# Kernel optimization log

Hardware: AMD Instinct MI355X
Metric: run time of the kernel (lower is better)

Reference implementation:

```python
import jax, jax.numpy as jnp
import numpy as np

B, Hm, Wm, Dm = 1, 32, 32, 32
N = Hm * Wm * Dm
C = 128
HEADS, DH = 8, 16
G = 32
L = 2
OUT = 1


def _ln(x, g, b):
    mu = jnp.mean(x, -1, keepdims=True)
    var = jnp.mean((x - mu) ** 2, -1, keepdims=True)
    return (x - mu) * jax.lax.rsqrt(var + 1e-5) * g + b


def setup_inputs() -> dict:
    key = jax.random.key(0)
    ks = iter(jax.random.split(key, 64))
    def nrm(shape, s=0.02):
        return jax.random.normal(next(ks), shape, jnp.float32) * s
    return {
        "x": jax.random.normal(next(ks), (B, N, 3), jnp.float32),
        "fx": jax.random.normal(next(ks), (B, N, 1), jnp.float32),
        "pre_w1": nrm((4, 2 * C)), "pre_b1": jnp.zeros((2 * C,), jnp.float32),
        "pre_w2": nrm((2 * C, C)), "pre_b2": jnp.zeros((C,), jnp.float32),
        "placeholder": jax.random.uniform(next(ks), (C,), jnp.float32) / C,
        "ln1_g": jnp.ones((L, C), jnp.float32), "ln1_b": jnp.zeros((L, C), jnp.float32),
        "convx_w": nrm((L, C, C, 3, 3, 3)), "convx_b": jnp.zeros((L, C), jnp.float32),
        "convfx_w": nrm((L, C, C, 3, 3, 3)), "convfx_b": jnp.zeros((L, C), jnp.float32),
        "slice_w": nrm((L, DH, G), 0.1), "slice_b": jnp.zeros((L, G), jnp.float32),
        "temperature": jnp.full((L, 1, HEADS, 1, 1), 0.5, jnp.float32),
        "wq": nrm((L, DH, DH), 0.1), "wk": nrm((L, DH, DH), 0.1), "wv": nrm((L, DH, DH), 0.1),
        "wo": nrm((L, HEADS * DH, C)), "bo": jnp.zeros((L, C), jnp.float32),
        "ln2_g": jnp.ones((L, C), jnp.float32), "ln2_b": jnp.zeros((L, C), jnp.float32),
        "mlp_w1": nrm((L, C, C)), "mlp_b1": jnp.zeros((L, C), jnp.float32),
        "mlp_w2": nrm((L, C, C)), "mlp_b2": jnp.zeros((L, C), jnp.float32),
        "ln3_g": jnp.ones((C,), jnp.float32), "ln3_b": jnp.zeros((C,), jnp.float32),
        "out_w": nrm((C, OUT)), "out_b": jnp.zeros((OUT,), jnp.float32),
    }


def _conv3d(x, w, b):
    # x: [B,C,H,W,D], w: [O,I,3,3,3], SAME padding (kernel//2) as torch Conv3d
    y = jax.lax.conv_general_dilated(x, w, (1, 1, 1), "SAME",
                                     dimension_numbers=("NCDHW", "OIDHW", "NCDHW"))
    return y + b[None, :, None, None, None]


def _physics_attn(z, cw_x, cb_x, cw_fx, cb_fx, sw, sb, temp, wq, wk, wv, wo, bo):
    # z: [B, N, C] -> structured mesh conv projections -> slice attention
    xg = z.reshape(B, Hm, Wm, Dm, C).transpose(0, 4, 1, 2, 3)  # [B,C,H,W,D]

    def split_heads(t):  # [B,I,H,W,D] -> [B,heads,N,dh]
        return t.transpose(0, 2, 3, 4, 1).reshape(B, N, HEADS, DH).transpose(0, 2, 1, 3)

    x_mid = split_heads(_conv3d(xg, cw_x, cb_x))
    fx_mid = split_heads(_conv3d(xg, cw_fx, cb_fx))
    # slice assignment weights: [B,heads,N,G], temperature-scaled softmax
    slice_logits = (x_mid @ sw + sb) / temp
    swt = jax.nn.softmax(slice_logits, axis=-1)
    norm = jnp.sum(swt, axis=2)  # [B,heads,G]
    tok = jnp.einsum("bhnc,bhng->bhgc", fx_mid, swt) / (norm + 1e-5)[..., None]
    q, k, v = tok @ wq, tok @ wk, tok @ wv  # [B,heads,G,dh]
    attn = jax.nn.softmax((q @ k.transpose(0, 1, 3, 2)) * (DH ** -0.5), axis=-1)
    ot = attn @ v  # [B,heads,G,dh]
    out = jnp.einsum("bhgc,bhng->bhnc", ot, swt)  # de-slice back to tokens
    out = out.transpose(0, 2, 1, 3).reshape(B, N, HEADS * DH)
    return out @ wo + bo


def reference(x, fx, pre_w1, pre_b1, pre_w2, pre_b2, placeholder,
              ln1_g, ln1_b, convx_w, convx_b, convfx_w, convfx_b,
              slice_w, slice_b, temperature, wq, wk, wv, wo, bo,
              ln2_g, ln2_b, mlp_w1, mlp_b1, mlp_w2, mlp_b2,
              ln3_g, ln3_b, out_w, out_b):
    h = jnp.concatenate([x, fx], axis=-1)  # [B,N,space+fun]
    z = jax.nn.gelu(h @ pre_w1 + pre_b1, approximate=False) @ pre_w2 + pre_b2 + placeholder
    for l in range(L):
        zn = _ln(z, ln1_g[l], ln1_b[l])
        z = _physics_attn(zn, convx_w[l], convx_b[l], convfx_w[l], convfx_b[l],
                          slice_w[l], slice_b[l], temperature[l],
                          wq[l], wk[l], wv[l], wo[l], bo[l]) + z
        zn = _ln(z, ln2_g[l], ln2_b[l])
        z = jax.nn.gelu(zn @ mlp_w1[l] + mlp_b1[l], approximate=False) @ mlp_w2[l] + mlp_b2[l] + z
    return _ln(z, ln3_g, ln3_b) @ out_w + out_b
```

## Files before the change

### kernel.cpp

```cpp
#include <hip/hip_runtime.h>
#include <hip/hip_bf16.h>

#define DEV __device__ __forceinline__

constexpr int N   = 32768;
constexpr int TOTAL_IN = 2038481;

constexpr int OFF_X        = 0;
constexpr int OFF_FX       = 98304;
constexpr int OFF_PRE_W1   = 131072;
constexpr int OFF_PRE_B1   = 132096;
constexpr int OFF_PRE_W2   = 132352;
constexpr int OFF_PRE_B2   = 165120;
constexpr int OFF_PLACE    = 165248;
constexpr int OFF_LN1_G    = 165376;
constexpr int OFF_LN1_B    = 165632;
constexpr int OFF_CONVX_W  = 165888;
constexpr int OFF_CONVX_B  = 1050624;
constexpr int OFF_CONVFX_W = 1050880;
constexpr int OFF_CONVFX_B = 1935616;
constexpr int OFF_SLICE_W  = 1935872;
constexpr int OFF_SLICE_B  = 1936896;
constexpr int OFF_TEMP     = 1936960;
constexpr int OFF_WQ       = 1936976;
constexpr int OFF_WK       = 1937488;
constexpr int OFF_WV       = 1938000;
constexpr int OFF_WO       = 1938512;
constexpr int OFF_BO       = 1971280;
constexpr int OFF_LN2_G    = 1971536;
constexpr int OFF_LN2_B    = 1971792;
constexpr int OFF_MLP_W1   = 1972048;
constexpr int OFF_MLP_B1   = 2004816;
constexpr int OFF_MLP_W2   = 2005072;
constexpr int OFF_MLP_B2   = 2037840;
constexpr int OFF_LN3_G    = 2038096;
constexpr int OFF_LN3_B    = 2038224;
constexpr int OFF_OUT_W    = 2038352;
constexpr int OFF_OUT_B    = 2038480;

__device__ __constant__ int d_PRE[32] = {
  0, 98304, 131072, 132096, 132352, 165120, 165248, 165376, 165632,
  165888, 1050624, 1050880, 1935616, 1935872, 1936896, 1936960, 1936976,
  1937488, 1938000, 1938512, 1971280, 1971536, 1971792, 1972048, 2004816,
  2005072, 2037840, 2038096, 2038224, 2038352, 2038480, 2038481
};

constexpr size_t F_IN   = 16;
constexpr size_t F_WT   = 2038512;
constexpr size_t F_Z    = F_WT   + 1769472;
constexpr size_t F_ZN   = F_Z    + 4194304;
constexpr size_t F_CONV = F_ZN   + 4194304;
constexpr size_t F_SWT  = F_CONV + 8388608;
constexpr size_t F_TOKP = F_SWT  + 8388608;
constexpr size_t F_TOK2 = F_TOKP + 1114112;
constexpr size_t F_OT   = F_TOK2 + 34816;
constexpr size_t F_WP   = F_OT   + 4096;
constexpr size_t F_END  = F_WP   + 65536;

struct InPtrs { const void* p[31]; };

typedef short short8v  __attribute__((ext_vector_type(8)));
typedef float float4v  __attribute__((ext_vector_type(4)));
#define MFMA16(A,B,C) __builtin_amdgcn_mfma_f32_16x16x32_bf16(A,B,C,0,0,0)

DEV float geluf(float x) { return 0.5f * x * (1.0f + erff(x * 0.70710678118654752f)); }
DEV short f2bs(float x) { union { __hip_bfloat16 h; short s; } c; c.h = __float2bfloat16(x); return c.s; }

__global__ void k_convert(InPtrs ptrs, float* __restrict__ ws) {
  const unsigned tw = *(const unsigned*)ptrs.p[15];
  const bool isbf = (tw == 0x3F003F00u);
  int stride = gridDim.x * blockDim.x;
  for (int e = blockIdx.x * blockDim.x + threadIdx.x; e < TOTAL_IN; e += stride) {
    if ((e >= OFF_CONVX_W && e < OFF_CONVX_B) || (e >= OFF_CONVFX_W && e < OFF_CONVFX_B)) continue;
    int lo = 0, hi = 30;
#pragma unroll
    for (int it = 0; it < 5; ++it) {
      int mid = (lo + hi + 1) >> 1;
      if (e >= d_PRE[mid]) lo = mid; else hi = mid - 1;
    }
    int loc = e - d_PRE[lo];
    float v;
    if (isbf) {
      unsigned short u = ((const unsigned short*)ptrs.p[lo])[loc];
      unsigned uu = ((unsigned)u) << 16;
      v = __uint_as_float(uu);
    } else {
      v = ((const float*)ptrs.p[lo])[loc];
    }
    ws[F_IN + e] = v;
  }
}

__global__ void k_wtrans(const void* __restrict__ cwxr, const void* __restrict__ cwfr,
                         const void* __restrict__ tempraw, short* __restrict__ wtf) {
  const bool isbf = (*(const unsigned*)tempraw == 0x3F003F00u);
  int f = blockIdx.x * 256 + threadIdx.x;
  if (f >= 221184) return;
  int lane = f & 63;
  int rest = f >> 6;
  int ntile = rest & 15;
  int r2 = rest >> 4;
  int layer = r2 / 108;
  int kt = r2 - layer * 108;
  int icb = kt / 27, tap = kt - icb * 27;
  int oc = ntile * 16 + (lane & 15);
  int ic0 = icb * 32 + (lane >> 4) * 8;
  const void* cw = (oc < 128) ? cwxr : cwfr;
  int o = oc & 127;
  size_t base = ((size_t)(layer * 128 + o) * 128) * 27 + tap;
  short8v out;
  if (isbf) {
    const unsigned short* src = (const unsigned short*)cw + base;
#pragma unroll
    for (int j = 0; j < 8; ++j) out[j] = (short)src[(size_t)(ic0 + j) * 27];
  } else {
    const float* src = (const float*)cw + base;
#pragma unroll
    for (int j = 0; j < 8; ++j) out[j] = f2bs(src[(size_t)(ic0 + j) * 27]);
  }
  *(short8v*)(wtf + (size_t)f * 8) = out;
}

__global__ void k_wpack(const float* __restrict__ ip, short* __restrict__ wp) {
  int f = blockIdx.x * 256 + threadIdx.x;
  if (f >= 16384) return;
  int lane = f & 63;
  int t = f >> 6;
  int srcoff, kt, nt;
  if (t < 64) { srcoff = OFF_PRE_W2; kt = t >> 3; nt = t & 7; }
  else {
    int r = t - 64, l = r / 96, r2 = r - l * 96;
    int which = r2 >> 5, idx2 = r2 & 31;
    kt = idx2 >> 3; nt = idx2 & 7;
    srcoff = (which == 0 ? OFF_MLP_W1 : (which == 1 ? OFF_MLP_W2 : OFF_WO)) + l * 16384;
  }
  int k0 = kt * 32 + (lane >> 4) * 8;
  int n = nt * 16 + (lane & 15);
  const float* src = ip + srcoff + (size_t)k0 * 128 + n;
  short8v out;
#pragma unroll
  for (int j = 0; j < 8; ++j) out[j] = f2bs(src[(size_t)j * 128]);
  *(short8v*)(wp + (size_t)f * 8) = out;
}

__global__ __launch_bounds__(256)
void k_prenet(const float* __restrict__ ip, const short* __restrict__ wp,
              float* __restrict__ z, short* __restrict__ znb) {
  __shared__ float w1s[1024], b1s[256], cvec[128], g1s[128], be1s[128];
  __shared__ float xv[64][4];
  __shared__ __align__(16) short ts[64 * 264];
  int tid = threadIdx.x;
  int wv = tid >> 6, lane = tid & 63;
  int m = lane & 15, q = lane >> 4;
  int n0 = blockIdx.x * 64;
  for (int i = tid; i < 1024; i += 256) w1s[i] = ip[OFF_PRE_W1 + i];
  b1s[tid] = ip[OFF_PRE_B1 + tid];
  if (tid < 128) {
    cvec[tid] = ip[OFF_PRE_B2 + tid] + ip[OFF_PLACE + tid];
    g1s[tid]  = ip[OFF_LN1_G + tid];
    be1s[tid] = ip[OFF_LN1_B + tid];
  }
  if (tid < 64) {
    xv[tid][0] = ip[OFF_X + (n0 + tid) * 3 + 0];
    xv[tid][1] = ip[OFF_X + (n0 + tid) * 3 + 1];
    xv[tid][2] = ip[OFF_X + (n0 + tid) * 3 + 2];
    xv[tid][3] = ip[OFF_FX + n0 + tid];
  }
  __syncthreads();
  {
    float w0 = w1s[tid], wA = w1s[256 + tid], wB = w1s[512 + tid], wC = w1s[768 + tid];
    float bb = b1s[tid];
    for (int t = 0; t < 64; ++t) {
      float hv = bb + xv[t][0] * w0 + xv[t][1] * wA + xv[t][2] * wB + xv[t][3] * wC;
      ts[t * 264 + tid] = f2bs(geluf(hv));
    }
  }
  __syncthreads();
  const short8v* pwf = (const short8v*)wp;
  float4v acc[8];
#pragma unroll
  for (int nt = 0; nt < 8; ++nt) acc[nt] = (float4v){0.f, 0.f, 0.f, 0.f};
  for (int kt = 0; kt < 8; ++kt) {
    short8v A = *(const short8v*)(ts + (wv * 16 + m) * 264 + kt * 32 + q * 8);
#pragma unroll
    for (int nt = 0; nt < 8; ++nt)
      acc[nt] = MFMA16(A, pwf[(kt * 8 + nt) * 64 + lane], acc[nt]);
  }
  float vz[8][4];
#pragma unroll
  for (int nt = 0; nt < 8; ++nt) {
    int col = nt * 16 + m;
#pragma unroll
    for (int r = 0; r < 4; ++r) {
      vz[nt][r] = acc[nt][r] + cvec[col];
      z[(size_t)(n0 + wv * 16 + q * 4 + r) * 128 + col] = vz[nt][r];
    }
  }
#pragma unroll
  for (int r = 0; r < 4; ++r) {
    float s1 = 0.f, s2 = 0.f;
#pragma unroll
    for (int nt = 0; nt < 8; ++nt) { float v = vz[nt][r]; s1 += v; s2 += v * v; }
#pragma unroll
    for (int off = 1; off < 16; off <<= 1) { s1 += __shfl_xor(s1, off); s2 += __shfl_xor(s2, off); }
    float mu = s1 * (1.0f / 128.0f);
    float var = s2 * (1.0f / 128.0f) - mu * mu;
    float rst = 1.0f / sqrtf(var + 1e-5f);
    size_t rowb = (size_t)(n0 + wv * 16 + q * 4 + r) * 128;
#pragma unroll
    for (int nt = 0; nt < 8; ++nt) {
      int col = nt * 16 + m;
      znb[rowb + col] = f2bs((vz[nt][r] - mu) * rst * g1s[col] + be1s[col]);
    }
  }
}

__global__ __launch_bounds__(512, 2)
void k_conv(const float* __restrict__ ip, const short* __restrict__ znb,
            const short* __restrict__ wtf, float* __restrict__ cv, int layer) {
  __shared__ __align__(16) short halo[19584];
  int tid = threadIdx.x;
  int wv = tid >> 6, lane = tid & 63;
  int m = lane & 15, q = lane >> 4;
  int half = wv >> 2, ocq = wv & 3;
  int n0 = blockIdx.x * 128;
  int h = n0 >> 10, w0 = (n0 >> 5) & 31;
  float bias_r[4];
#pragma unroll
  for (int nt = 0; nt < 4; ++nt) {
    int oc = (ocq * 4 + nt) * 16 + m;
    bias_r[nt] = (oc < 128) ? ip[OFF_CONVX_B + layer * 128 + oc]
                            : ip[OFF_CONVFX_B + layer * 128 + (oc - 128)];
  }
  float4v acc[4][4];
#pragma unroll
  for (int a = 0; a < 4; ++a)
#pragma unroll
    for (int b = 0; b < 4; ++b) acc[a][b] = (float4v){0.f, 0.f, 0.f, 0.f};

  const short8v* wf = (const short8v*)wtf + (size_t)layer * 110592 + (ocq * 4) * 64 + lane;
  const short* hq = halo + q * 4896;
  const int rowA = half * 2;
  short8v bc0 = wf[0], bc1 = wf[64], bc2 = wf[128], bc3 = wf[192];
  short8v A0, A1, A2, A3;

  for (int icb = 0; icb < 4; ++icb) {
    __syncthreads();
    for (int pr = tid; pr < 612; pr += 512) {
      int line = pr / 34, dpos = pr - line * 34;
      int lh = line / 6, lw = line - lh * 6;
      int hh2 = h + lh - 1, ww2 = w0 + lw - 1, dd2 = dpos - 1;
      bool ok = ((unsigned)hh2 < 32u) && ((unsigned)ww2 < 32u) && ((unsigned)dd2 < 32u);
      int tok = (hh2 << 10) + (ww2 << 5) + dd2;
#pragma unroll
      for (int qq = 0; qq < 4; ++qq) {
        short8v v = (short8v){0, 0, 0, 0, 0, 0, 0, 0};
        if (ok) v = *(const short8v*)(znb + (size_t)tok * 128 + icb * 32 + qq * 8);
        *(short8v*)(halo + qq * 4896 + pr * 8) = v;
      }
    }
    __syncthreads();
    {
      const short* hp = hq + (rowA * 34 + m) * 8;
      A0 = *(const short8v*)(hp);
      A1 = *(const short8v*)(hp + 128);
      A2 = *(const short8v*)(hp + 272);
      A3 = *(const short8v*)(hp + 400);
    }
    int ktb = icb * 27;
    for (int tap = 0; tap < 27; ++tap) {
      int kt = ktb + tap;
      int ktn = (kt + 1 < 108) ? kt + 1 : kt;
      const short8v* wn = wf + (size_t)ktn * 1024;
      short8v bn0 = wn[0], bn1 = wn[64], bn2 = wn[128], bn3 = wn[192];
      short8v An0, An1, An2, An3;
      if (tap < 26) {
        int tp = tap + 1;
        int ta = tp / 9, rem = tp - ta * 9, tb = rem / 3, tc = rem - tb * 3;
        const short* hp = hq + (((ta * 6 + rowA + tb) * 34) + tc + m) * 8;
        An0 = *(const short8v*)(hp);
        An1 = *(const short8v*)(hp + 128);
        An2 = *(const short8v*)(hp + 272);
        An3 = *(const short8v*)(hp + 400);
      }
      acc[0][0] = MFMA16(A0, bc0, acc[0][0]);
      acc[1][0] = MFMA16(A1, bc0, acc[1][0]);
      acc[2][0] = MFMA16(A2, bc0, acc[2][0]);
      acc[3][0] = MFMA16(A3, bc0, acc[3][0]);
      acc[0][1] = MFMA16(A0, bc1, acc[0][1]);
      acc[1][1] = MFMA16(A1, bc1, acc[1][1]);
      acc[2][1] = MFMA16(A2, bc1, acc[2][1]);
      acc[3][1] = MFMA16(A3, bc1, acc[3][1]);
      acc[0][2] = MFMA16(A0, bc2, acc[0][2]);
      acc[1][2] = MFMA16(A1, bc2, acc[1][2]);
      acc[2][2] = MFMA16(A2, bc2, acc[2][2]);
      acc[3][2] = MFMA16(A3, bc2, acc[3][2]);
      acc[0][3] = MFMA16(A0, bc3, acc[0][3]);
      acc[1][3] = MFMA16(A1, bc3, acc[1][3]);
      acc[2][3] = MFMA16(A2, bc3, acc[2][3]);
      acc[3][3] = MFMA16(A3, bc3, acc[3][3]);
      bc0 = bn0; bc1 = bn1; bc2 = bn2; bc3 = bn3;
      if (tap < 26) { A0 = An0; A1 = An1; A2 = An2; A3 = An3; }
    }
  }
#pragma unroll
  for (int mt = 0; mt < 4; ++mt) {
    float* cp = cv + (size_t)(n0 + half * 64 + mt * 16 + q * 4) * 256 + (ocq * 4) * 16 + m;
#pragma unroll
    for (int nt = 0; nt < 4; ++nt) {
#pragma unroll
      for (int r = 0; r < 4; ++r)
        cp[(size_t)r * 256 + nt * 16] = acc[mt][nt][r] + bias_r[nt];
    }
  }
}

__global__ __launch_bounds__(256)
void k_slice(const float* __restrict__ ip, const float* __restrict__ cv,
             short* __restrict__ swtb, float* __restrict__ tokp, int layer) {
  __shared__ float sws[512], sbs[32], its[8];
  __shared__ float swl[32 * 257];
  __shared__ float fxl[32 * 128];
  int tid = threadIdx.x;
  for (int i = tid; i < 512; i += 256) sws[i] = ip[OFF_SLICE_W + layer * 512 + i];
  if (tid < 32) sbs[tid] = ip[OFF_SLICE_B + layer * 32 + tid];
  if (tid < 8)  its[tid] = 1.0f / ip[OFF_TEMP + layer * 8 + tid];
  float4 ta0 = make_float4(0,0,0,0), ta1 = ta0, ta2 = ta0, ta3 = ta0;
  float np = 0.f;
  for (int s = 0; s < 4; ++s) {
    int tbase = blockIdx.x * 128 + s * 32;
    __syncthreads();
    for (int i = tid; i < 1024; i += 256) {
      int t = i >> 5, c4 = (i & 31) * 4;
      *(float4*)&fxl[t * 128 + c4] = *(const float4*)&cv[(size_t)(tbase + t) * 256 + 128 + c4];
    }
    {
      int t = tid >> 3, hh = tid & 7;
      float xm[16];
#pragma unroll
      for (int qq = 0; qq < 4; ++qq)
        *(float4*)&xm[qq * 4] = *(const float4*)&cv[(size_t)(tbase + t) * 256 + hh * 16 + qq * 4];
      float lg[32];
      float itv = its[hh];
#pragma unroll
      for (int g = 0; g < 32; ++g) {
        float sacc = sbs[g];
#pragma unroll
        for (int j = 0; j < 16; ++j) sacc += xm[j] * sws[j * 32 + g];
        lg[g] = sacc * itv;
      }
      float mx = -1e30f;
#pragma unroll
      for (int g = 0; g < 32; ++g) mx = fmaxf(mx, lg[g]);
      float sum = 0.f;
#pragma unroll
      for (int g = 0; g < 32; ++g) { lg[g] = expf(lg[g] - mx); sum += lg[g]; }
      float inv = 1.0f / sum;
#pragma unroll
      for (int g = 0; g < 32; ++g) {
        lg[g] *= inv;
        swl[t * 257 + hh * 32 + g] = lg[g];
      }
#pragma unroll
      for (int qq = 0; qq < 4; ++qq) {
        short8v pk;
#pragma unroll
        for (int j = 0; j < 8; ++j) pk[j] = f2bs(lg[qq * 8 + j]);
        *(short8v*)(swtb + (size_t)(tbase + t) * 256 + hh * 32 + qq * 8) = pk;
      }
    }
    __syncthreads();
    {
      int ah = tid >> 5, ag = tid & 31;
      for (int t2 = 0; t2 < 32; ++t2) {
        float sv = swl[t2 * 257 + ah * 32 + ag];
        np += sv;
        const float* f = &fxl[t2 * 128 + ah * 16];
        float4 f0 = *(const float4*)&f[0], f1 = *(const float4*)&f[4];
        float4 f2 = *(const float4*)&f[8], f3 = *(const float4*)&f[12];
        ta0.x += sv * f0.x; ta0.y += sv * f0.y; ta0.z += sv * f0.z; ta0.w += sv * f0.w;
        ta1.x += sv * f1.x; ta1.y += sv * f1.y; ta1.z += sv * f1.z; ta1.w += sv * f1.w;
        ta2.x += sv * f2.x; ta2.y += sv * f2.y; ta2.z += sv * f2.z; ta2.w += sv * f2.w;
        ta3.x += sv * f3.x; ta3.y += sv * f3.y; ta3.z += sv * f3.z; ta3.w += sv * f3.w;
      }
    }
  }
  int ah = tid >> 5, ag = tid & 31;
  size_t base = (size_t)blockIdx.x * 4352 + (size_t)(ah * 32 + ag) * 16;
  *(float4*)&tokp[base + 0]  = ta0;
  *(float4*)&tokp[base + 4]  = ta1;
  *(float4*)&tokp[base + 8]  = ta2;
  *(float4*)&tokp[base + 12] = ta3;
  tokp[(size_t)blockIdx.x * 4352 + 4096 + ah * 32 + ag] = np;
}

__global__ void k_tokred1(const float* __restrict__ tokp, float* __restrict__ tok2) {
  int ogrp = blockIdx.x % 17, bgrp = blockIdx.x / 17;
  int o = ogrp * 256 + threadIdx.x;
  float s = 0.f;
  int b0 = bgrp * 32;
#pragma unroll 8
  for (int b = b0; b < b0 + 32; ++b) s += tokp[(size_t)b * 4352 + o];
  tok2[(size_t)bgrp * 4352 + o] = s;
}

__global__ __launch_bounds__(256)
void k_fused(const float* __restrict__ ip, const short* __restrict__ swtb,
             const float* __restrict__ tok2, const short* __restrict__ wp,
             float* __restrict__ z, short* __restrict__ znb,
             void* __restrict__ dout, const void* __restrict__ tempraw, int layer) {
  __shared__ __align__(16) char smem[64512];
  short* otb = (short*)smem;
  float* bia = (float*)(smem + 8192);
  float* trs = (float*)(smem + 12288);
  short* znt = (short*)(smem + 12288);
  float* kk  = (float*)(smem + 29696);
  short* al  = (short*)(smem + 29696);
  float* vvs = (float*)(smem + 47104);
  float* bol = bia, *b1s = bia + 128, *b2s = bia + 256, *g2s = bia + 384;
  float* be2s = bia + 512, *lng = bia + 640, *lnb = bia + 768, *ows = bia + 896;
  int tid = threadIdx.x;
  int wv = tid >> 6, lane = tid & 63;
  int m = lane & 15, q = lane >> 4;
  int n0 = blockIdx.x * 64;
  if (tid < 128) {
    bol[tid]  = ip[OFF_BO + layer * 128 + tid];
    b1s[tid]  = ip[OFF_MLP_B1 + layer * 128 + tid];
    b2s[tid]  = ip[OFF_MLP_B2 + layer * 128 + tid];
    g2s[tid]  = ip[OFF_LN2_G + layer * 128 + tid];
    be2s[tid] = ip[OFF_LN2_B + layer * 128 + tid];
    if (layer == 0) {
      lng[tid] = ip[OFF_LN1_G + 128 + tid];
      lnb[tid] = ip[OFF_LN1_B + 128 + tid];
      ows[tid] = 0.f;
    } else {
      lng[tid] = ip[OFF_LN3_G + tid];
      lnb[tid] = ip[OFF_LN3_B + tid];
      ows[tid] = ip[OFF_OUT_W + tid];
    }
  }
  for (int i = tid; i < 4352; i += 256) {
    float s = 0.f;
#pragma unroll
    for (int b = 0; b < 8; ++b) s += tok2[(size_t)b * 4352 + i];
    trs[i] = s;
  }
  __syncthreads();
  float qv[16];
  {
    const float* wqp = ip + OFF_WQ + layer * 256;
    const float* wkp = ip + OFF_WK + layer * 256;
    const float* wvp = ip + OFF_WV + layer * 256;
    float inv = 1.0f / (trs[4096 + tid] + 1e-5f);
    float t[16];
#pragma unroll
    for (int c = 0; c < 16; ++c) t[c] = trs[tid * 16 + c] * inv;
#pragma unroll
    for (int c = 0; c < 16; ++c) {
      float aq = 0.f, ak = 0.f, av = 0.f;
#pragma unroll
      for (int j = 0; j < 16; ++j) {
        float tv = t[j];
        aq += tv * wqp[j * 16 + c];
        ak += tv * wkp[j * 16 + c];
        av += tv * wvp[j * 16 + c];
      }
      qv[c] = aq;
      kk[tid * 17 + c] = ak;
      vvs[tid * 17 + c] = av;
    }
  }
  __syncthreads();
  {
    int hh = tid >> 5, g = tid & 31;
    float sc[32];
    float mx = -1e30f;
#pragma unroll
    for (int g2 = 0; g2 < 32; ++g2) {
      float s = 0.f;
#pragma unroll
      for (int c = 0; c < 16; ++c) s += qv[c] * kk[(hh * 32 + g2) * 17 + c];
      s *= 0.25f;
      sc[g2] = s; mx = fmaxf(mx, s);
    }
    float sum = 0.f;
#pragma unroll
    for (int g2 = 0; g2 < 32; ++g2) { sc[g2] = expf(sc[g2] - mx); sum += sc[g2]; }
    float inv2 = 1.0f / sum;
    float o[16];
#pragma unroll
    for (int c = 0; c < 16; ++c) o[c] = 0.f;
#pragma unroll
    for (int g2 = 0; g2 < 32; ++g2) {
      float p = sc[g2] * inv2;
#pragma unroll
      for (int c = 0; c < 16; ++c) o[c] += p * vvs[(hh * 32 + g2) * 17 + c];
    }
#pragma unroll
    for (int dh = 0; dh < 16; ++dh)
      otb[hh * 512 + (((g >> 3) * 16 + dh) << 3) + (g & 7)] = f2bs(o[dh]);
  }
  __syncthreads();
  float4v accd[8];
#pragma unroll
  for (int h = 0; h < 8; ++h) accd[h] = (float4v){0.f, 0.f, 0.f, 0.f};
#pragma unroll
  for (int h = 0; h < 8; ++h) {
    short8v A = *(const short8v*)(swtb + (size_t)(n0 + wv * 16 + m) * 256 + h * 32 + q * 8);
    accd[h] = MFMA16(A, *(const short8v*)(otb + h * 512 + lane * 8), accd[h]);
  }
  __syncthreads();
#pragma unroll
  for (int h = 0; h < 8; ++h)
#pragma unroll
    for (int r = 0; r < 4; ++r)
      al[(wv * 16 + q * 4 + r) * 136 + h * 16 + m] = f2bs(accd[h][r]);
  __syncthreads();
  const short8v* wof = (const short8v*)(wp + (size_t)(128 + 96 * layer) * 512);
  float4v a2[8];
#pragma unroll
  for (int nt = 0; nt < 8; ++nt) a2[nt] = (float4v){0.f, 0.f, 0.f, 0.f};
  for (int kt = 0; kt < 4; ++kt) {
    short8v A = *(const short8v*)(al + (wv * 16 + m) * 136 + kt * 32 + q * 8);
#pragma unroll
    for (int nt = 0; nt < 8; ++nt)
      a2[nt] = MFMA16(A, wof[(kt * 8 + nt) * 64 + lane], a2[nt]);
  }
  float vmid[8][4];
#pragma unroll
  for (int nt = 0; nt < 8; ++nt) {
    int col = nt * 16 + m;
#pragma unroll
    for (int r = 0; r < 4; ++r)
      vmid[nt][r] = z[(size_t)(n0 + wv * 16 + q * 4 + r) * 128 + col] + a2[nt][r] + bol[col];
  }
#pragma unroll
  for (int r = 0; r < 4; ++r) {
    float s1 = 0.f, s2 = 0.f;
#pragma unroll
    for (int nt = 0; nt < 8; ++nt) { float v = vmid[nt][r]; s1 += v; s2 += v * v; }
#pragma unroll
    for (int off = 1; off < 16; off <<= 1) { s1 += __shfl_xor(s1, off); s2 += __shfl_xor(s2, off); }
    float mu = s1 * (1.0f / 128.0f);
    float var = s2 * (1.0f / 128.0f) - mu * mu;
    float rst = 1.0f / sqrtf(var + 1e-5f);
#pragma unroll
    for (int nt = 0; nt < 8; ++nt) {
      int col = nt * 16 + m;
      znt[(wv * 16 + q * 4 + r) * 136 + col] = f2bs((vmid[nt][r] - mu) * rst * g2s[col] + be2s[col]);
    }
  }
  __syncthreads();
  const short8v* w1f = (const short8v*)(wp + (size_t)(64 + 96 * layer) * 512);
  const short8v* w2f = (const short8v*)(wp + (size_t)(96 + 96 * layer) * 512);
  float4v acc[8];
#pragma unroll
  for (int nt = 0; nt < 8; ++nt) acc[nt] = (float4v){0.f, 0.f, 0.f, 0.f};
  for (int kt = 0; kt < 4; ++kt) {
    short8v A = *(const short8v*)(znt + (wv * 16 + m) * 136 + kt * 32 + q * 8);
#pragma unroll
    for (int nt = 0; nt < 8; ++nt)
      acc[nt] = MFMA16(A, w1f[(kt * 8 + nt) * 64 + lane], acc[nt]);
  }
  __syncthreads();
#pragma unroll
  for (int nt = 0; nt < 8; ++nt) {
    int col = nt * 16 + m;
#pragma unroll
    for (int r = 0; r < 4; ++r)
      al[(wv * 16 + q * 4 + r) * 136 + col] = f2bs(geluf(acc[nt][r] + b1s[col]));
  }
  __syncthreads();
  float4v a4[8];
#pragma unroll
  for (int nt = 0; nt < 8; ++nt) a4[nt] = (float4v){0.f, 0.f, 0.f, 0.f};
  for (int kt = 0; kt < 4; ++kt) {
    short8v A = *(const short8v*)(al + (wv * 16 + m) * 136 + kt * 32 + q * 8);
#pragma unroll
    for (int nt = 0; nt < 8; ++nt)
      a4[nt] = MFMA16(A, w2f[(kt * 8 + nt) * 64 + lane], a4[nt]);
  }
  float vfin[8][4];
#pragma unroll
  for (int nt = 0; nt < 8; ++nt) {
    int col = nt * 16 + m;
#pragma unroll
    for (int r = 0; r < 4; ++r) {
      vfin[nt][r] = vmid[nt][r] + a4[nt][r] + b2s[col];
      z[(size_t)(n0 + wv * 16 + q * 4 + r) * 128 + col] = vfin[nt][r];
    }
  }
#pragma unroll
  for (int r = 0; r < 4; ++r) {
    float s1 = 0.f, s2 = 0.f;
#pragma unroll
    for (int nt = 0; nt < 8; ++nt) { float v = vfin[nt][r]; s1 += v; s2 += v * v; }
#pragma unroll
    for (int off = 1; off < 16; off <<= 1) { s1 += __shfl_xor(s1, off); s2 += __shfl_xor(s2, off); }
    float mu = s1 * (1.0f / 128.0f);
    float var = s2 * (1.0f / 128.0f) - mu * mu;
    float rst = 1.0f / sqrtf(var + 1e-5f);
    int n = n0 + wv * 16 + q * 4 + r;
    if (layer == 0) {
      size_t rowb = (size_t)n * 128;
#pragma unroll
      for (int nt = 0; nt < 8; ++nt) {
        int col = nt * 16 + m;
        znb[rowb + col] = f2bs((vfin[nt][r] - mu) * rst * lng[col] + lnb[col]);
      }
    } else {
      float contrib = 0.f;
#pragma unroll
      for (int nt = 0; nt < 8; ++nt) {
        int col = nt * 16 + m;
        contrib += ((vfin[nt][r] - mu) * rst * lng[col] + lnb[col]) * ows[col];
      }
#pragma unroll
      for (int off = 1; off < 16; off <<= 1) contrib += __shfl_xor(contrib, off);
      if (m == 0) {
        float res = contrib + ip[OFF_OUT_B];
        unsigned tw = *(const unsigned*)tempraw;
        if (tw == 0x3F003F00u) ((__hip_bfloat16*)dout)[n] = __float2bfloat16(res);
        else                   ((float*)dout)[n] = res;
      }
    }
  }
}

extern "C" void kernel_launch(void* const* d_in, const int* in_sizes, int n_in,
                              void* d_out, int out_size, void* d_ws, size_t ws_size,
                              hipStream_t stream) {
  (void)in_sizes; (void)out_size; (void)ws_size;
  if (n_in < 31) return;
  float* ws   = (float*)d_ws;
  float* ip   = ws + F_IN;
  short* wtf  = (short*)(ws + F_WT);
  float* z    = ws + F_Z;
  short* znb  = (short*)(ws + F_ZN);
  float* cv   = ws + F_CONV;
  short* swtb = (short*)(ws + F_SWT);
  float* tkp  = ws + F_TOKP;
  float* tk2  = ws + F_TOK2;
  short* wp   = (short*)(ws + F_WP);

  InPtrs P;
  for (int i = 0; i < 31; ++i) P.p[i] = d_in[i];

  k_convert<<<512, 256, 0, stream>>>(P, ws);
  k_wtrans <<<864, 256, 0, stream>>>(d_in[9], d_in[11], d_in[15], wtf);
  k_wpack  <<<64, 256, 0, stream>>>(ip, wp);
  k_prenet <<<512, 256, 0, stream>>>(ip, wp, z, znb);
  for (int l = 0; l < 2; ++l) {
    k_conv   <<<256, 512, 0, stream>>>(ip, znb, wtf, cv, l);
    k_slice  <<<256, 256, 0, stream>>>(ip, cv, swtb, tkp, l);
    k_tokred1<<<136, 256, 0, stream>>>(tkp, tk2);
    k_fused  <<<512, 256, 0, stream>>>(ip, swtb, tk2, wp, z, znb, d_out, d_in[15], l);
  }
}
```

Measured before the change: 487.8 us.

## Merge setup kernels, shrink conv tiles, replace token reduction with atomics

Three setup kernels (convert, conv-weight transpose, weight pack) are merged into one launch, and the weight pack now reads the raw inputs directly. The conv kernel moves from 512-thread blocks covering 128 tokens to 256-thread blocks covering 64 tokens, with a smaller halo and no software prefetch of the A fragments. The slice kernel now accumulates its token partials straight into a global buffer with atomicAdd, which the conv kernel zeroes, so the separate two-stage reduction kernel is removed. This cuts launches and intermediate traffic, but adds atomic contention, float-order nondeterminism and a smaller per-block conv tile.

```diff
diff --git a/kernel.cpp b/kernel.cpp
--- a/kernel.cpp
+++ b/kernel.cpp
@@ -51,10 +51,8 @@
 constexpr size_t F_ZN   = F_Z    + 4194304;
 constexpr size_t F_CONV = F_ZN   + 4194304;
 constexpr size_t F_SWT  = F_CONV + 8388608;
-constexpr size_t F_TOKP = F_SWT  + 8388608;
-constexpr size_t F_TOK2 = F_TOKP + 1114112;
-constexpr size_t F_OT   = F_TOK2 + 34816;
-constexpr size_t F_WP   = F_OT   + 4096;
+constexpr size_t F_TOKR = F_SWT  + 8388608;
+constexpr size_t F_WP   = F_TOKR + 4608;
 constexpr size_t F_END  = F_WP   + 65536;
 
 struct InPtrs { const void* p[31]; };
@@ -66,81 +64,83 @@
 DEV float geluf(float x) { return 0.5f * x * (1.0f + erff(x * 0.70710678118654752f)); }
 DEV short f2bs(float x) { union { __hip_bfloat16 h; short s; } c; c.h = __float2bfloat16(x); return c.s; }
 
-__global__ void k_convert(InPtrs ptrs, float* __restrict__ ws) {
-  const unsigned tw = *(const unsigned*)ptrs.p[15];
-  const bool isbf = (tw == 0x3F003F00u);
-  int stride = gridDim.x * blockDim.x;
-  for (int e = blockIdx.x * blockDim.x + threadIdx.x; e < TOTAL_IN; e += stride) {
-    if ((e >= OFF_CONVX_W && e < OFF_CONVX_B) || (e >= OFF_CONVFX_W && e < OFF_CONVFX_B)) continue;
-    int lo = 0, hi = 30;
-#pragma unroll
-    for (int it = 0; it < 5; ++it) {
-      int mid = (lo + hi + 1) >> 1;
-      if (e >= d_PRE[mid]) lo = mid; else hi = mid - 1;
-    }
-    int loc = e - d_PRE[lo];
-    float v;
+__global__ void k_setup(InPtrs ptrs, float* __restrict__ ws,
+                        short* __restrict__ wtf, short* __restrict__ wp) {
+  const bool isbf = (*(const unsigned*)ptrs.p[15] == 0x3F003F00u);
+  int b = blockIdx.x, tid = threadIdx.x;
+  if (b < 512) {
+    int stride = 512 * 256;
+    for (int e = b * 256 + tid; e < TOTAL_IN; e += stride) {
+      if ((e >= OFF_CONVX_W && e < OFF_CONVX_B) || (e >= OFF_CONVFX_W && e < OFF_CONVFX_B)) continue;
+      int lo = 0, hi = 30;
+#pragma unroll
+      for (int it = 0; it < 5; ++it) {
+        int mid = (lo + hi + 1) >> 1;
+        if (e >= d_PRE[mid]) lo = mid; else hi = mid - 1;
+      }
+      int loc = e - d_PRE[lo];
+      float v;
+      if (isbf) {
+        unsigned short u = ((const unsigned short*)ptrs.p[lo])[loc];
+        v = __uint_as_float(((unsigned)u) << 16);
+      } else {
+        v = ((const float*)ptrs.p[lo])[loc];
+      }
+      ws[F_IN + e] = v;
+    }
+  } else if (b < 1376) {
+    int f = (b - 512) * 256 + tid;
+    int lane = f & 63;
+    int rest = f >> 6;
+    int ntile = rest & 15;
+    int r2 = rest >> 4;
+    int layer = r2 / 108;
+    int kt = r2 - layer * 108;
+    int icb = kt / 27, tap = kt - icb * 27;
+    int oc = ntile * 16 + (lane & 15);
+    int ic0 = icb * 32 + (lane >> 4) * 8;
+    const void* cw = (oc < 128) ? ptrs.p[9] : ptrs.p[11];
+    int o = oc & 127;
+    size_t base = ((size_t)(layer * 128 + o) * 128) * 27 + tap;
+    short8v out;
     if (isbf) {
-      unsigned short u = ((const unsigned short*)ptrs.p[lo])[loc];
-      unsigned uu = ((unsigned)u) << 16;
-      v = __uint_as_float(uu);
+      const unsigned short* src = (const unsigned short*)cw + base;
+#pragma unroll
+      for (int j = 0; j < 8; ++j) out[j] = (short)src[(size_t)(ic0 + j) * 27];
     } else {
-      v = ((const float*)ptrs.p[lo])[loc];
-    }
-    ws[F_IN + e] = v;
-  }
-}
-
-__global__ void k_wtrans(const void* __restrict__ cwxr, const void* __restrict__ cwfr,
-                         const void* __restrict__ tempraw, short* __restrict__ wtf) {
-  const bool isbf = (*(const unsigned*)tempraw == 0x3F003F00u);
-  int f = blockIdx.x * 256 + threadIdx.x;
-  if (f >= 221184) return;
-  int lane = f & 63;
-  int rest = f >> 6;
-  int ntile = rest & 15;
-  int r2 = rest >> 4;
-  int layer = r2 / 108;
-  int kt = r2 - layer * 108;
-  int icb = kt / 27, tap = kt - icb * 27;
-  int oc = ntile * 16 + (lane & 15);
-  int ic0 = icb * 32 + (lane >> 4) * 8;
-  const void* cw = (oc < 128) ? cwxr : cwfr;
-  int o = oc & 127;
-  size_t base = ((size_t)(layer * 128 + o) * 128) * 27 + tap;
-  short8v out;
-  if (isbf) {
-    const unsigned short* src = (const unsigned short*)cw + base;
-#pragma unroll
-    for (int j = 0; j < 8; ++j) out[j] = (short)src[(size_t)(ic0 + j) * 27];
+      const float* src = (const float*)cw + base;
+#pragma unroll
+      for (int j = 0; j < 8; ++j) out[j] = f2bs(src[(size_t)(ic0 + j) * 27]);
+    }
+    *(short8v*)(wtf + (size_t)f * 8) = out;
   } else {
-    const float* src = (const float*)cw + base;
-#pragma unroll
-    for (int j = 0; j < 8; ++j) out[j] = f2bs(src[(size_t)(ic0 + j) * 27]);
-  }
-  *(short8v*)(wtf + (size_t)f * 8) = out;
-}
-
-__global__ void k_wpack(const float* __restrict__ ip, short* __restrict__ wp) {
-  int f = blockIdx.x * 256 + threadIdx.x;
-  if (f >= 16384) return;
-  int lane = f & 63;
-  int t = f >> 6;
-  int srcoff, kt, nt;
-  if (t < 64) { srcoff = OFF_PRE_W2; kt = t >> 3; nt = t & 7; }
-  else {
-    int r = t - 64, l = r / 96, r2 = r - l * 96;
-    int which = r2 >> 5, idx2 = r2 & 31;
-    kt = idx2 >> 3; nt = idx2 & 7;
-    srcoff = (which == 0 ? OFF_MLP_W1 : (which == 1 ? OFF_MLP_W2 : OFF_WO)) + l * 16384;
-  }
-  int k0 = kt * 32 + (lane >> 4) * 8;
-  int n = nt * 16 + (lane & 15);
-  const float* src = ip + srcoff + (size_t)k0 * 128 + n;
-  short8v out;
-#pragma unroll
-  for (int j = 0; j < 8; ++j) out[j] = f2bs(src[(size_t)j * 128]);
-  *(short8v*)(wp + (size_t)f * 8) = out;
+    int f = (b - 1376) * 256 + tid;
+    int lane = f & 63;
+    int t = f >> 6;
+    const void* srcb; size_t soff; int kt, nt;
+    if (t < 64) { srcb = ptrs.p[4]; soff = 0; kt = t >> 3; nt = t & 7; }
+    else {
+      int r = t - 64, l = r / 96, r2 = r - l * 96;
+      int which = r2 >> 5, idx2 = r2 & 31;
+      kt = idx2 >> 3; nt = idx2 & 7;
+      srcb = (which == 0 ? ptrs.p[23] : (which == 1 ? ptrs.p[25] : ptrs.p[19]));
+      soff = (size_t)l * 16384;
+    }
+    int k0 = kt * 32 + (lane >> 4) * 8;
+    int n = nt * 16 + (lane & 15);
+    size_t base = soff + (size_t)k0 * 128 + n;
+    short8v out;
+    if (isbf) {
+      const unsigned short* src = (const unsigned short*)srcb + base;
+#pragma unroll
+      for (int j = 0; j < 8; ++j) out[j] = (short)src[(size_t)j * 128];
+    } else {
+      const float* src = (const float*)srcb + base;
+#pragma unroll
+      for (int j = 0; j < 8; ++j) out[j] = f2bs(src[(size_t)j * 128]);
+    }
+    *(short8v*)(wp + (size_t)f * 8) = out;
+  }
 }
 
 __global__ __launch_bounds__(256)
@@ -215,20 +215,22 @@
   }
 }
 
-__global__ __launch_bounds__(512, 2)
+__global__ __launch_bounds__(256)
 void k_conv(const float* __restrict__ ip, const short* __restrict__ znb,
-            const short* __restrict__ wtf, float* __restrict__ cv, int layer) {
-  __shared__ __align__(16) short halo[19584];
+            const short* __restrict__ wtf, float* __restrict__ cv,
+            float* __restrict__ tokr, int layer) {
+  __shared__ __align__(16) short halo[15360];
   int tid = threadIdx.x;
+  int gz = blockIdx.x * 256 + tid;
+  if (gz < 4352) tokr[gz] = 0.f;
   int wv = tid >> 6, lane = tid & 63;
   int m = lane & 15, q = lane >> 4;
-  int half = wv >> 2, ocq = wv & 3;
-  int n0 = blockIdx.x * 128;
+  int n0 = blockIdx.x * 64;
   int h = n0 >> 10, w0 = (n0 >> 5) & 31;
   float bias_r[4];
 #pragma unroll
   for (int nt = 0; nt < 4; ++nt) {
-    int oc = (ocq * 4 + nt) * 16 + m;
+    int oc = (wv * 4 + nt) * 16 + m;
     bias_r[nt] = (oc < 128) ? ip[OFF_CONVX_B + layer * 128 + oc]
                             : ip[OFF_CONVFX_B + layer * 128 + (oc - 128)];
   }
@@ -238,74 +240,60 @@
 #pragma unroll
     for (int b = 0; b < 4; ++b) acc[a][b] = (float4v){0.f, 0.f, 0.f, 0.f};
 
-  const short8v* wf = (const short8v*)wtf + (size_t)layer * 110592 + (ocq * 4) * 64 + lane;
-  const short* hq = halo + q * 4896;
-  const int rowA = half * 2;
+  const short8v* wf = (const short8v*)wtf + (size_t)layer * 110592 + (wv * 4) * 64 + lane;
   short8v bc0 = wf[0], bc1 = wf[64], bc2 = wf[128], bc3 = wf[192];
-  short8v A0, A1, A2, A3;
-
-  for (int icb = 0; icb < 4; ++icb) {
-    __syncthreads();
-    for (int pr = tid; pr < 612; pr += 512) {
-      int line = pr / 34, dpos = pr - line * 34;
-      int lh = line / 6, lw = line - lh * 6;
-      int hh2 = h + lh - 1, ww2 = w0 + lw - 1, dd2 = dpos - 1;
-      bool ok = ((unsigned)hh2 < 32u) && ((unsigned)ww2 < 32u) && ((unsigned)dd2 < 32u);
-      int tok = (hh2 << 10) + (ww2 << 5) + dd2;
-#pragma unroll
-      for (int qq = 0; qq < 4; ++qq) {
+
+  int tap = 0, icb = 0;
+  for (int kt = 0; kt < 108; ++kt) {
+    if (tap == 0) {
+      __syncthreads();
+      for (int i = tid; i < 1632; i += 256) {
+        int pr = i >> 2, qq = i & 3;
+        int line = pr / 34, dpos = pr - line * 34;
+        int hh2 = h + (line >> 2) - 1, ww2 = w0 + (line & 3) - 1, dd2 = dpos - 1;
         short8v v = (short8v){0, 0, 0, 0, 0, 0, 0, 0};
-        if (ok) v = *(const short8v*)(znb + (size_t)tok * 128 + icb * 32 + qq * 8);
-        *(short8v*)(halo + qq * 4896 + pr * 8) = v;
-      }
-    }
-    __syncthreads();
-    {
-      const short* hp = hq + (rowA * 34 + m) * 8;
-      A0 = *(const short8v*)(hp);
-      A1 = *(const short8v*)(hp + 128);
-      A2 = *(const short8v*)(hp + 272);
-      A3 = *(const short8v*)(hp + 400);
-    }
-    int ktb = icb * 27;
-    for (int tap = 0; tap < 27; ++tap) {
-      int kt = ktb + tap;
-      int ktn = (kt + 1 < 108) ? kt + 1 : kt;
-      const short8v* wn = wf + (size_t)ktn * 1024;
-      short8v bn0 = wn[0], bn1 = wn[64], bn2 = wn[128], bn3 = wn[192];
-      short8v An0, An1, An2, An3;
-      if (tap < 26) {
-        int tp = tap + 1;
-        int ta = tp / 9, rem = tp - ta * 9, tb = rem / 3, tc = rem - tb * 3;
-        const short* hp = hq + (((ta * 6 + rowA + tb) * 34) + tc + m) * 8;
-        An0 = *(const short8v*)(hp);
-        An1 = *(const short8v*)(hp + 128);
-        An2 = *(const short8v*)(hp + 272);
-        An3 = *(const short8v*)(hp + 400);
-      }
-      acc[0][0] = MFMA16(A0, bc0, acc[0][0]);
-      acc[1][0] = MFMA16(A1, bc0, acc[1][0]);
-      acc[2][0] = MFMA16(A2, bc0, acc[2][0]);
-      acc[3][0] = MFMA16(A3, bc0, acc[3][0]);
-      acc[0][1] = MFMA16(A0, bc1, acc[0][1]);
-      acc[1][1] = MFMA16(A1, bc1, acc[1][1]);
-      acc[2][1] = MFMA16(A2, bc1, acc[2][1]);
-      acc[3][1] = MFMA16(A3, bc1, acc[3][1]);
-      acc[0][2] = MFMA16(A0, bc2, acc[0][2]);
-      acc[1][2] = MFMA16(A1, bc2, acc[1][2]);
-      acc[2][2] = MFMA16(A2, bc2, acc[2][2]);
-      acc[3][2] = MFMA16(A3, bc2, acc[3][2]);
-      acc[0][3] = MFMA16(A0, bc3, acc[0][3]);
-      acc[1][3] = MFMA16(A1, bc3, acc[1][3]);
-      acc[2][3] = MFMA16(A2, bc3, acc[2][3]);
-      acc[3][3] = MFMA16(A3, bc3, acc[3][3]);
-      bc0 = bn0; bc1 = bn1; bc2 = bn2; bc3 = bn3;
-      if (tap < 26) { A0 = An0; A1 = An1; A2 = An2; A3 = An3; }
-    }
+        if (((unsigned)hh2 < 32u) && ((unsigned)ww2 < 32u) && ((unsigned)dd2 < 32u)) {
+          int tok = (hh2 << 10) + (ww2 << 5) + dd2;
+          v = *(const short8v*)(znb + (size_t)tok * 128 + icb * 32 + qq * 8);
+        }
+        *(short8v*)(halo + qq * 3840 + (line * 40 + dpos) * 8) = v;
+      }
+      __syncthreads();
+    }
+    int ktn = (kt + 1 < 108) ? kt + 1 : kt;
+    const short8v* wn = wf + (size_t)ktn * 1024;
+    short8v bn0 = wn[0], bn1 = wn[64], bn2 = wn[128], bn3 = wn[192];
+
+    int ta = tap / 9, rem = tap - ta * 9, tb = rem / 3, tc = rem - tb * 3;
+    const short* hp = halo + q * 3840 + ((ta * 4 + tb) * 40 + tc + m) * 8;
+    short8v A0 = *(const short8v*)(hp);
+    short8v A1 = *(const short8v*)(hp + 128);
+    short8v A2 = *(const short8v*)(hp + 320);
+    short8v A3 = *(const short8v*)(hp + 448);
+
+    acc[0][0] = MFMA16(A0, bc0, acc[0][0]);
+    acc[1][0] = MFMA16(A1, bc0, acc[1][0]);
+    acc[2][0] = MFMA16(A2, bc0, acc[2][0]);
+    acc[3][0] = MFMA16(A3, bc0, acc[3][0]);
+    acc[0][1] = MFMA16(A0, bc1, acc[0][1]);
+    acc[1][1] = MFMA16(A1, bc1, acc[1][1]);
+    acc[2][1] = MFMA16(A2, bc1, acc[2][1]);
+    acc[3][1] = MFMA16(A3, bc1, acc[3][1]);
+    acc[0][2] = MFMA16(A0, bc2, acc[0][2]);
+    acc[1][2] = MFMA16(A1, bc2, acc[1][2]);
+    acc[2][2] = MFMA16(A2, bc2, acc[2][2]);
+    acc[3][2] = MFMA16(A3, bc2, acc[3][2]);
+    acc[0][3] = MFMA16(A0, bc3, acc[0][3]);
+    acc[1][3] = MFMA16(A1, bc3, acc[1][3]);
+    acc[2][3] = MFMA16(A2, bc3, acc[2][3]);
+    acc[3][3] = MFMA16(A3, bc3, acc[3][3]);
+
+    bc0 = bn0; bc1 = bn1; bc2 = bn2; bc3 = bn3;
+    if (++tap == 27) { tap = 0; ++icb; }
   }
 #pragma unroll
   for (int mt = 0; mt < 4; ++mt) {
-    float* cp = cv + (size_t)(n0 + half * 64 + mt * 16 + q * 4) * 256 + (ocq * 4) * 16 + m;
+    float* cp = cv + (size_t)(n0 + mt * 16 + q * 4) * 256 + (wv * 4) * 16 + m;
 #pragma unroll
     for (int nt = 0; nt < 4; ++nt) {
 #pragma unroll
@@ -317,7 +305,7 @@
 
 __global__ __launch_bounds__(256)
 void k_slice(const float* __restrict__ ip, const float* __restrict__ cv,
-             short* __restrict__ swtb, float* __restrict__ tokp, int layer) {
+             short* __restrict__ swtb, float* __restrict__ tokr, int layer) {
   __shared__ float sws[512], sbs[32], its[8];
   __shared__ float swl[32 * 257];
   __shared__ float fxl[32 * 128];
@@ -327,8 +315,8 @@
   if (tid < 8)  its[tid] = 1.0f / ip[OFF_TEMP + layer * 8 + tid];
   float4 ta0 = make_float4(0,0,0,0), ta1 = ta0, ta2 = ta0, ta3 = ta0;
   float np = 0.f;
-  for (int s = 0; s < 4; ++s) {
-    int tbase = blockIdx.x * 128 + s * 32;
+  for (int s = 0; s < 2; ++s) {
+    int tbase = blockIdx.x * 64 + s * 32;
     __syncthreads();
     for (int i = tid; i < 1024; i += 256) {
       int t = i >> 5, c4 = (i & 31) * 4;
@@ -386,27 +374,17 @@
     }
   }
   int ah = tid >> 5, ag = tid & 31;
-  size_t base = (size_t)blockIdx.x * 4352 + (size_t)(ah * 32 + ag) * 16;
-  *(float4*)&tokp[base + 0]  = ta0;
-  *(float4*)&tokp[base + 4]  = ta1;
-  *(float4*)&tokp[base + 8]  = ta2;
-  *(float4*)&tokp[base + 12] = ta3;
-  tokp[(size_t)blockIdx.x * 4352 + 4096 + ah * 32 + ag] = np;
-}
-
-__global__ void k_tokred1(const float* __restrict__ tokp, float* __restrict__ tok2) {
-  int ogrp = blockIdx.x % 17, bgrp = blockIdx.x / 17;
-  int o = ogrp * 256 + threadIdx.x;
-  float s = 0.f;
-  int b0 = bgrp * 32;
-#pragma unroll 8
-  for (int b = b0; b < b0 + 32; ++b) s += tokp[(size_t)b * 4352 + o];
-  tok2[(size_t)bgrp * 4352 + o] = s;
+  float* tr = tokr + (ah * 32 + ag) * 16;
+  atomicAdd(&tr[0],  ta0.x); atomicAdd(&tr[1],  ta0.y); atomicAdd(&tr[2],  ta0.z); atomicAdd(&tr[3],  ta0.w);
+  atomicAdd(&tr[4],  ta1.x); atomicAdd(&tr[5],  ta1.y); atomicAdd(&tr[6],  ta1.z); atomicAdd(&tr[7],  ta1.w);
+  atomicAdd(&tr[8],  ta2.x); atomicAdd(&tr[9],  ta2.y); atomicAdd(&tr[10], ta2.z); atomicAdd(&tr[11], ta2.w);
+  atomicAdd(&tr[12], ta3.x); atomicAdd(&tr[13], ta3.y); atomicAdd(&tr[14], ta3.z); atomicAdd(&tr[15], ta3.w);
+  atomicAdd(&tokr[4096 + ah * 32 + ag], np);
 }
 
 __global__ __launch_bounds__(256)
 void k_fused(const float* __restrict__ ip, const short* __restrict__ swtb,
-             const float* __restrict__ tok2, const short* __restrict__ wp,
+             const float* __restrict__ tokr, const short* __restrict__ wp,
              float* __restrict__ z, short* __restrict__ znb,
              void* __restrict__ dout, const void* __restrict__ tempraw, int layer) {
   __shared__ __align__(16) char smem[64512];
@@ -439,12 +417,7 @@
       ows[tid] = ip[OFF_OUT_W + tid];
     }
   }
-  for (int i = tid; i < 4352; i += 256) {
-    float s = 0.f;
-#pragma unroll
-    for (int b = 0; b < 8; ++b) s += tok2[(size_t)b * 4352 + i];
-    trs[i] = s;
-  }
+  for (int i = tid; i < 4352; i += 256) trs[i] = tokr[i];
   __syncthreads();
   float qv[16];
   {
@@ -639,21 +612,17 @@
   short* znb  = (short*)(ws + F_ZN);
   float* cv   = ws + F_CONV;
   short* swtb = (short*)(ws + F_SWT);
-  float* tkp  = ws + F_TOKP;
-  float* tk2  = ws + F_TOK2;
+  float* tkr  = ws + F_TOKR;
   short* wp   = (short*)(ws + F_WP);
 
   InPtrs P;
   for (int i = 0; i < 31; ++i) P.p[i] = d_in[i];
 
-  k_convert<<<512, 256, 0, stream>>>(P, ws);
-  k_wtrans <<<864, 256, 0, stream>>>(d_in[9], d_in[11], d_in[15], wtf);
-  k_wpack  <<<64, 256, 0, stream>>>(ip, wp);
-  k_prenet <<<512, 256, 0, stream>>>(ip, wp, z, znb);
+  k_setup <<<1440, 256, 0, stream>>>(P, ws, wtf, wp);
+  k_prenet<<<512, 256, 0, stream>>>(ip, wp, z, znb);
   for (int l = 0; l < 2; ++l) {
-    k_conv   <<<256, 512, 0, stream>>>(ip, znb, wtf, cv, l);
-    k_slice  <<<256, 256, 0, stream>>>(ip, cv, swtb, tkp, l);
-    k_tokred1<<<136, 256, 0, stream>>>(tkp, tk2);
-    k_fused  <<<512, 256, 0, stream>>>(ip, swtb, tk2, wp, z, znb, d_out, d_in[15], l);
+    k_conv <<<512, 256, 0, stream>>>(ip, znb, wtf, cv, tkr, l);
+    k_slice<<<512, 256, 0, stream>>>(ip, cv, swtb, tkr, l);
+    k_fused<<<512, 256, 0, stream>>>(ip, swtb, tkr, wp, z, znb, d_out, d_in[15], l);
   }
 }
```

Result: slower. 832.1 us (+70.6%).
